# Kernel optimization log

Hardware: AMD Instinct MI355X
Metric: run time of the kernel (lower is better)

Reference implementation:

```python
import jax, jax.numpy as jnp
import numpy as np

N_NODES = 100000
N_EDGES = 1600000
IN_DIM = 128
HID = 64
HEADS = 1
NEG_SLOPE = 0.2


def setup_inputs() -> dict:
    key = jax.random.key(0)
    ks = jax.random.split(key, 12)
    def xavier(k, shape):
        fan_in, fan_out = shape[-2], shape[-1]
        lim = jnp.sqrt(6.0 / (fan_in + fan_out))
        return jax.random.uniform(k, shape, jnp.float32, -lim, lim)
    x = jax.random.normal(ks[0], (N_NODES, IN_DIM), jnp.float32)
    edge_index = jax.random.randint(ks[1], (2, N_EDGES), 0, N_NODES, jnp.int64)
    # layer 0: in 128 -> heads*hid (64)
    W0 = xavier(ks[2], (IN_DIM, HEADS * HID))
    al0 = xavier(ks[3], (1, HEADS, HID))
    ar0 = xavier(ks[4], (1, HEADS, HID))
    # layer 1: in heads*hid (64) -> 64
    W1 = xavier(ks[5], (HEADS * HID, HEADS * HID))
    al1 = xavier(ks[6], (1, HEADS, HID))
    ar1 = xavier(ks[7], (1, HEADS, HID))
    # post_mp: Linear(64,64) -> Linear(64,64)
    Wp1 = xavier(ks[8], (HEADS * HID, HID))
    bp1 = jnp.zeros((HID,), jnp.float32)
    Wp2 = xavier(ks[9], (HID, HID))
    bp2 = jnp.zeros((HID,), jnp.float32)
    return {"x": x, "edge_index": edge_index, "W0": W0, "al0": al0, "ar0": ar0,
            "W1": W1, "al1": al1, "ar1": ar1, "Wp1": Wp1, "bp1": bp1,
            "Wp2": Wp2, "bp2": bp2}


def gat_layer(x, W, att_l, att_r, src, dst, n_nodes):
    H, C = att_l.shape[1], att_l.shape[2]
    # lin_l == lin_r (shared weight), no bias
    xh = (x @ W).reshape(n_nodes, H, C)            # [N,H,C]
    alpha_l = jnp.sum(xh * att_l, axis=-1)         # [N,H]
    alpha_r = jnp.sum(xh * att_r, axis=-1)         # [N,H]
    # per-edge logit: alpha_i (dst) + alpha_j (src)
    a = alpha_l[src] + alpha_r[dst]                # [E,H]
    a = jnp.where(a >= 0, a, NEG_SLOPE * a)        # leaky_relu
    # segment softmax over incoming edges of each dst node
    amax = jax.ops.segment_max(a, dst, num_segments=n_nodes)
    e = jnp.exp(a - amax[dst])
    denom = jax.ops.segment_sum(e, dst, num_segments=n_nodes)
    alpha = e / (denom[dst] + 1e-16)               # [E,H]
    msg = xh[src] * alpha[:, :, None]              # [E,H,C]
    out = jax.ops.segment_sum(msg, dst, num_segments=n_nodes)  # [N,H,C]
    return out.reshape(n_nodes, H * C)


def reference(x, edge_index, W0, al0, ar0, W1, al1, ar1, Wp1, bp1, Wp2, bp2):
    src, dst = edge_index[0], edge_index[1]
    n = x.shape[0]
    h = gat_layer(x, W0, al0, ar0, src, dst, n)
    h = jax.nn.relu(h)
    h = gat_layer(h, W1, al1, ar1, src, dst, n)
    h = jax.nn.relu(h)
    # post_mp (dropout inactive in eval)
    h = h @ Wp1 + bp1
    h = h @ Wp2 + bp2
    return h  # emb=True -> return embedding
```

## Files before the change

### kernel.cpp

```cpp
#include <hip/hip_runtime.h>
#include <math.h>

#define NEG_SLOPE 0.2f
#define CAP 8192

typedef _Float16 half8 __attribute__((ext_vector_type(8)));
typedef _Float16 half4v __attribute__((ext_vector_type(4)));
typedef float float4v __attribute__((ext_vector_type(4)));

__global__ void init_cursor(int* __restrict__ cursor, int NB) {
    int i = blockIdx.x * blockDim.x + threadIdx.x;
    if (i < NB) cursor[i] = i * CAP;
}

__global__ void prep_wt(const float* __restrict__ W0, const float* __restrict__ W1,
                        const float* __restrict__ Wp1, const float* __restrict__ Wp2,
                        _Float16* __restrict__ W0T, _Float16* __restrict__ W1T,
                        _Float16* __restrict__ Wp1T, _Float16* __restrict__ Wp2T) {
    __shared__ float lds[128 * 64];
    const float* src; _Float16* dstp; int K;
    switch (blockIdx.x) {
        case 0: src = W0;  dstp = W0T;  K = 128; break;
        case 1: src = W1;  dstp = W1T;  K = 64;  break;
        case 2: src = Wp1; dstp = Wp1T; K = 64;  break;
        default: src = Wp2; dstp = Wp2T; K = 64; break;
    }
    const int tid = threadIdx.x;
    for (int i = tid; i < K * 64; i += 256) lds[i] = src[i];
    __syncthreads();
    for (int i = tid; i < K * 64; i += 256) {
        int n = i / K, k = i % K;
        dstp[i] = (_Float16)lds[k * 64 + n];
    }
}


__global__ void bucket_bin(const int* __restrict__ src, const int* __restrict__ dst,
                           int* __restrict__ cursor, unsigned int* __restrict__ packed,
                           int E, int NB) {
    __shared__ int h[512];
    const int tid = threadIdx.x;
    for (int t = tid; t < NB; t += 256) h[t] = 0;
    __syncthreads();
    const int base = blockIdx.x * 4096;
    const int lim = min(base + 4096, E);
    for (int i = base + tid; i < lim; i += 256)
        atomicAdd(&h[dst[i] >> 8], 1);
    __syncthreads();
    for (int t = tid; t < NB; t += 256) {
        int c = h[t];
        h[t] = c ? atomicAdd(&cursor[t], c) : 0;
    }
    __syncthreads();
    for (int i = base + tid; i < lim; i += 256) {
        int d = dst[i];
        int pos = atomicAdd(&h[d >> 8], 1);
        packed[pos] = ((unsigned int)(d & 255) << 24) | (unsigned int)src[i];
    }
}

__global__ void bucket_sort(const unsigned int* __restrict__ packed,
                            const int* __restrict__ cursor,
                            int* __restrict__ csr, int* __restrict__ rbeg,
                            int* __restrict__ rend, int N) {
    __shared__ int hist[256], cur[256];
    __shared__ int wsum[4], woff[4];
    const int tid = threadIdx.x, wid = tid >> 6, lane = tid & 63;
    const int b = blockIdx.x;
    const int beg = b * CAP;
    const int end = cursor[b];
    hist[tid] = 0;
    __syncthreads();
    for (int i = beg + tid; i < end; i += 256)
        atomicAdd(&hist[packed[i] >> 24], 1);
    __syncthreads();
    int v = hist[tid];
    int x = v;
    #pragma unroll
    for (int off = 1; off < 64; off <<= 1) {
        int t = __shfl_up(x, off);
        if (lane >= off) x += t;
    }
    if (lane == 63) wsum[wid] = x;
    __syncthreads();
    if (tid == 0) {
        int acc = 0;
        #pragma unroll
        for (int w = 0; w < 4; ++w) { woff[w] = acc; acc += wsum[w]; }
    }
    __syncthreads();
    int excl = woff[wid] + x - v;
    int node = (b << 8) + tid;
    if (node < N) { rbeg[node] = beg + excl; rend[node] = beg + excl + v; }
    cur[tid] = excl;
    __syncthreads();
    for (int i = beg + tid; i < end; i += 256) {
        unsigned int p = packed[i];
        int pos = atomicAdd(&cur[p >> 24], 1);
        csr[beg + pos] = (int)(p & 0xFFFFFFu);
    }
}

template<int K, bool RELU>
__global__ void gemm_node_mfma(const float* __restrict__ X,
                               const _Float16* __restrict__ WT,
                               const float* __restrict__ alw, const float* __restrict__ arw,
                               _Float16* __restrict__ XH, float* __restrict__ AL,
                               float* __restrict__ AR, int N) {
    const int wid = threadIdx.x >> 6, lane = threadIdx.x & 63;
    const int rowbase = blockIdx.x * 64 + wid * 16;
    const int idx16 = lane & 15;
    const int g = lane >> 4;
    const int mrow = rowbase + idx16;
    const bool mvalid = (mrow < N);

    float4v acc[4];
    #pragma unroll
    for (int n = 0; n < 4; ++n) acc[n] = float4v{0.f, 0.f, 0.f, 0.f};

    #pragma unroll
    for (int ks = 0; ks < K / 32; ++ks) {
        const int k0 = ks * 32 + g * 8;
        half8 a = {};
        if (mvalid) {
            const float* xp = X + (size_t)mrow * K + k0;
            float4v lo = *reinterpret_cast<const float4v*>(xp);
            float4v hi = *reinterpret_cast<const float4v*>(xp + 4);
            #pragma unroll
            for (int i = 0; i < 4; ++i) {
                float l = RELU ? fmaxf(lo[i], 0.f) : lo[i];
                float h = RELU ? fmaxf(hi[i], 0.f) : hi[i];
                a[i] = (_Float16)l;
                a[i + 4] = (_Float16)h;
            }
        }
        #pragma unroll
        for (int n = 0; n < 4; ++n) {
            const half8 b = *reinterpret_cast<const half8*>(WT + (size_t)(n * 16 + idx16) * K + k0);
            acc[n] = __builtin_amdgcn_mfma_f32_16x16x32_f16(a, b, acc[n], 0, 0, 0);
        }
    }

    float alv[4], arv[4];
    #pragma unroll
    for (int n = 0; n < 4; ++n) { alv[n] = alw[n * 16 + idx16]; arv[n] = arw[n * 16 + idx16]; }
    #pragma unroll
    for (int r = 0; r < 4; ++r) {
        const int row = rowbase + g * 4 + r;
        if (row < N) {
            float pl = 0.f, pr = 0.f;
            #pragma unroll
            for (int n = 0; n < 4; ++n) {
                float vv = acc[n][r];
                XH[(size_t)row * 64 + n * 16 + idx16] = (_Float16)vv;
                pl = fmaf(vv, alv[n], pl);
                pr = fmaf(vv, arv[n], pr);
            }
            pl += __shfl_xor(pl, 1); pr += __shfl_xor(pr, 1);
            pl += __shfl_xor(pl, 2); pr += __shfl_xor(pr, 2);
            pl += __shfl_xor(pl, 4); pr += __shfl_xor(pr, 4);
            pl += __shfl_xor(pl, 8); pr += __shfl_xor(pr, 8);
            if (idx16 == 0) { AL[row] = pl; AR[row] = pr; }
        }
    }
}


__device__ __forceinline__ void agg_phase(const int* __restrict__ rbeg,
                                          const int* __restrict__ rend,
                                          const int* __restrict__ csr,
                                          const float* __restrict__ ALp,
                                          const float* __restrict__ ARp,
                                          const _Float16* __restrict__ XHp,
                                          _Float16* ts, int nb, int N) {
    const int tid = threadIdx.x;
    const int l = tid & 15, grp = tid >> 4;
    const int node = nb + grp;
    float4v acc = {0.f, 0.f, 0.f, 0.f};
    float inv = 0.0f;
    if (node < N) {
        const int beg = rbeg[node], end = rend[node];
        const float ar = ARp[node];
        float s = 0.f;
        for (int cbeg = beg; cbeg < end; cbeg += 16) {
            const int e = cbeg + l;
            const bool valid = (e < end);
            const int sidx = valid ? csr[e] : 0;
            float a = ALp[sidx] + ar;
            a = (a >= 0.0f) ? a : NEG_SLOPE * a;
            const float ex = valid ? __expf(a) : 0.0f;
            s += ex;
            #pragma unroll
            for (int j = 0; j < 16; ++j) {
                const float wgt = __shfl(ex, j, 16);
                const int si = __shfl(sidx, j, 16);
                const half4v h = *reinterpret_cast<const half4v*>(XHp + (size_t)si * 64 + l * 4);
                acc[0] = fmaf((float)h[0], wgt, acc[0]);
                acc[1] = fmaf((float)h[1], wgt, acc[1]);
                acc[2] = fmaf((float)h[2], wgt, acc[2]);
                acc[3] = fmaf((float)h[3], wgt, acc[3]);
            }
        }
        s += __shfl_xor(s, 1); s += __shfl_xor(s, 2);
        s += __shfl_xor(s, 4); s += __shfl_xor(s, 8);
        inv = 1.0f / (s + 1e-16f);
    }
    half4v o;
    o[0] = (_Float16)fmaxf(acc[0] * inv, 0.f);
    o[1] = (_Float16)fmaxf(acc[1] * inv, 0.f);
    o[2] = (_Float16)fmaxf(acc[2] * inv, 0.f);
    o[3] = (_Float16)fmaxf(acc[3] * inv, 0.f);
    const int hoff = (grp * 128 + ((l * 8) ^ ((grp & 7) << 4))) >> 1;
    *reinterpret_cast<half4v*>(ts + hoff) = o;
    __syncthreads();
}

__device__ __forceinline__ half8 ts_afrag(const _Float16* ts, int row, int kb) {
    return *reinterpret_cast<const half8*>(ts + ((row * 128 + (kb ^ ((row & 7) << 4))) >> 1));
}

__global__ void agg_gemm_mid(const int* __restrict__ rbeg, const int* __restrict__ rend,
                             const int* __restrict__ csr,
                             const float* __restrict__ AL0, const float* __restrict__ AR0,
                             const _Float16* __restrict__ XH0,
                             const _Float16* __restrict__ W1T,
                             const float* __restrict__ al1w, const float* __restrict__ ar1w,
                             _Float16* __restrict__ XH1, float* __restrict__ AL1,
                             float* __restrict__ AR1, int N) {
    __shared__ _Float16 ts[16 * 64];
    const int nb = blockIdx.x * 16;
    agg_phase(rbeg, rend, csr, AL0, AR0, XH0, ts, nb, N);
    if (threadIdx.x >= 64) return;

    const int lane = threadIdx.x;
    const int idx16 = lane & 15, g = lane >> 4;
    float alv[4], arv[4];
    #pragma unroll
    for (int n = 0; n < 4; ++n) { alv[n] = al1w[n * 16 + idx16]; arv[n] = ar1w[n * 16 + idx16]; }

    float4v acc[4];
    #pragma unroll
    for (int n = 0; n < 4; ++n) acc[n] = float4v{0.f, 0.f, 0.f, 0.f};
    #pragma unroll
    for (int ks = 0; ks < 2; ++ks) {
        const half8 a = ts_afrag(ts, idx16, ks * 64 + g * 16);
        const int k0 = ks * 32 + g * 8;
        #pragma unroll
        for (int n = 0; n < 4; ++n) {
            const half8 b = *reinterpret_cast<const half8*>(W1T + (size_t)(n * 16 + idx16) * 64 + k0);
            acc[n] = __builtin_amdgcn_mfma_f32_16x16x32_f16(a, b, acc[n], 0, 0, 0);
        }
    }
    #pragma unroll
    for (int r = 0; r < 4; ++r) {
        const int row = nb + g * 4 + r;
        if (row < N) {
            float pl = 0.f, pr = 0.f;
            #pragma unroll
            for (int n = 0; n < 4; ++n) {
                float vv = acc[n][r];
                XH1[(size_t)row * 64 + n * 16 + idx16] = (_Float16)vv;
                pl = fmaf(vv, alv[n], pl);
                pr = fmaf(vv, arv[n], pr);
            }
            pl += __shfl_xor(pl, 1); pr += __shfl_xor(pr, 1);
            pl += __shfl_xor(pl, 2); pr += __shfl_xor(pr, 2);
            pl += __shfl_xor(pl, 4); pr += __shfl_xor(pr, 4);
            pl += __shfl_xor(pl, 8); pr += __shfl_xor(pr, 8);
            if (idx16 == 0) { AL1[row] = pl; AR1[row] = pr; }
        }
    }
}

__global__ void agg_post(const int* __restrict__ rbeg, const int* __restrict__ rend,
                         const int* __restrict__ csr,
                         const float* __restrict__ AL1, const float* __restrict__ AR1,
                         const _Float16* __restrict__ XH1,
                         const _Float16* __restrict__ Wp1T, const float* __restrict__ bp1,
                         const _Float16* __restrict__ Wp2T, const float* __restrict__ bp2,
                         float* __restrict__ OUT, int N) {
    __shared__ _Float16 ts[16 * 64];
    __shared__ _Float16 tls[16][72];
    const int nb = blockIdx.x * 16;
    agg_phase(rbeg, rend, csr, AL1, AR1, XH1, ts, nb, N);
    if (threadIdx.x >= 64) return;

    const int lane = threadIdx.x;
    const int idx16 = lane & 15, g = lane >> 4;

    float4v acc1[4];
    #pragma unroll
    for (int n = 0; n < 4; ++n) acc1[n] = float4v{0.f, 0.f, 0.f, 0.f};
    #pragma unroll
    for (int ks = 0; ks < 2; ++ks) {
        const half8 a = ts_afrag(ts, idx16, ks * 64 + g * 16);
        const int k0 = ks * 32 + g * 8;
        #pragma unroll
        for (int n = 0; n < 4; ++n) {
            const half8 b = *reinterpret_cast<const half8*>(Wp1T + (size_t)(n * 16 + idx16) * 64 + k0);
            acc1[n] = __builtin_amdgcn_mfma_f32_16x16x32_f16(a, b, acc1[n], 0, 0, 0);
        }
    }
    #pragma unroll
    for (int r = 0; r < 4; ++r)
        #pragma unroll
        for (int n = 0; n < 4; ++n)
            tls[g * 4 + r][n * 16 + idx16] = (_Float16)(acc1[n][r] + bp1[n * 16 + idx16]);

    float4v acc2[4];
    #pragma unroll
    for (int n = 0; n < 4; ++n) acc2[n] = float4v{0.f, 0.f, 0.f, 0.f};
    #pragma unroll
    for (int ks = 0; ks < 2; ++ks) {
        const int k0 = ks * 32 + g * 8;
        const half8 a = *reinterpret_cast<const half8*>(&tls[idx16][k0]);
        #pragma unroll
        for (int n = 0; n < 4; ++n) {
            const half8 b = *reinterpret_cast<const half8*>(Wp2T + (size_t)(n * 16 + idx16) * 64 + k0);
            acc2[n] = __builtin_amdgcn_mfma_f32_16x16x32_f16(a, b, acc2[n], 0, 0, 0);
        }
    }
    #pragma unroll
    for (int r = 0; r < 4; ++r) {
        const int row = nb + g * 4 + r;
        if (row < N) {
            #pragma unroll
            for (int n = 0; n < 4; ++n)
                OUT[(size_t)row * 64 + n * 16 + idx16] = acc2[n][r] + bp2[n * 16 + idx16];
        }
    }
}

extern "C" void kernel_launch(void* const* d_in, const int* in_sizes, int n_in,
                              void* d_out, int out_size, void* d_ws, size_t ws_size,
                              hipStream_t stream) {
    const float* x   = (const float*)d_in[0];
    const int*   ei  = (const int*)d_in[1];
    const float* W0  = (const float*)d_in[2];
    const float* al0 = (const float*)d_in[3];
    const float* ar0 = (const float*)d_in[4];
    const float* W1  = (const float*)d_in[5];
    const float* al1 = (const float*)d_in[6];
    const float* ar1 = (const float*)d_in[7];
    const float* Wp1 = (const float*)d_in[8];
    const float* bp1 = (const float*)d_in[9];
    const float* Wp2 = (const float*)d_in[10];
    const float* bp2 = (const float*)d_in[11];
    float* out = (float*)d_out;

    const int N = in_sizes[0] / 128;
    const int E = in_sizes[1] / 2;
    const int* src = ei;
    const int* dst = ei + E;
    const int NB = (N + 255) >> 8;

    char* w = (char*)d_ws;
    _Float16* XH0  = (_Float16*)w;     w += sizeof(_Float16) * (size_t)N * 64;
    _Float16* XH1  = (_Float16*)w;     w += sizeof(_Float16) * (size_t)N * 64;
    float*  AL0    = (float*)w;        w += sizeof(float) * N;
    float*  AR0    = (float*)w;        w += sizeof(float) * N;
    float*  AL1    = (float*)w;        w += sizeof(float) * N;
    float*  AR1    = (float*)w;        w += sizeof(float) * N;
    int*    rbeg   = (int*)w;          w += sizeof(int) * N;
    int*    rend   = (int*)w;          w += sizeof(int) * N;
    int*    csr    = (int*)w;          w += sizeof(int) * (size_t)NB * CAP;
    unsigned int* packed = (unsigned int*)w; w += sizeof(unsigned int) * (size_t)NB * CAP;
    int*    cursor = (int*)w;          w += sizeof(int) * 512;
    _Float16* W0T  = (_Float16*)w;     w += sizeof(_Float16) * 128 * 64;
    _Float16* W1T  = (_Float16*)w;     w += sizeof(_Float16) * 64 * 64;
    _Float16* Wp1T = (_Float16*)w;     w += sizeof(_Float16) * 64 * 64;
    _Float16* Wp2T = (_Float16*)w;

    dim3 blk(256);
    const int gn64 = (N + 63) / 64;
    const int gn16 = (N + 15) / 16;
    const int geb  = (E + 4095) / 4096;

    prep_wt<<<4, blk, 0, stream>>>(W0, W1, Wp1, Wp2, W0T, W1T, Wp1T, Wp2T);
    init_cursor<<<2, blk, 0, stream>>>(cursor, NB);
    bucket_bin<<<geb, blk, 0, stream>>>(src, dst, cursor, packed, E, NB);
    bucket_sort<<<NB, blk, 0, stream>>>(packed, cursor, csr, rbeg, rend, N);

    gemm_node_mfma<128, false><<<gn64, blk, 0, stream>>>(x, W0T, al0, ar0, XH0, AL0, AR0, N);

    agg_gemm_mid<<<gn16, blk, 0, stream>>>(rbeg, rend, csr, AL0, AR0, XH0,
                                           W1T, al1, ar1, XH1, AL1, AR1, N);

    agg_post<<<gn16, blk, 0, stream>>>(rbeg, rend, csr, AL1, AR1, XH1,
                                       Wp1T, bp1, Wp2T, bp2, out, N);
}
```

Measured before the change: 162.9 us.

## Fuse setup kernels and co-schedule edge binning with layer-0 GEMM

Merges cursor init into the weight-transpose kernel. The edge bucket-binning pass and the layer-0 node GEMM now share a single launch, split by block index, so the two independent phases run concurrently and the launch count drops. Binning caches dst indices in registers rather than reading them twice. Row begin/end offsets are packed into one int2 array so each node needs one load. The risk is added register pressure from the dreg array and uneven block mixing within the fused launch.

```diff
diff --git a/kernel.cpp b/kernel.cpp
--- a/kernel.cpp
+++ b/kernel.cpp
@@ -8,15 +8,16 @@
 typedef _Float16 half4v __attribute__((ext_vector_type(4)));
 typedef float float4v __attribute__((ext_vector_type(4)));
 
-__global__ void init_cursor(int* __restrict__ cursor, int NB) {
-    int i = blockIdx.x * blockDim.x + threadIdx.x;
-    if (i < NB) cursor[i] = i * CAP;
-}
-
-__global__ void prep_wt(const float* __restrict__ W0, const float* __restrict__ W1,
-                        const float* __restrict__ Wp1, const float* __restrict__ Wp2,
-                        _Float16* __restrict__ W0T, _Float16* __restrict__ W1T,
-                        _Float16* __restrict__ Wp1T, _Float16* __restrict__ Wp2T) {
+__global__ void setup_misc(const float* __restrict__ W0, const float* __restrict__ W1,
+                           const float* __restrict__ Wp1, const float* __restrict__ Wp2,
+                           _Float16* __restrict__ W0T, _Float16* __restrict__ W1T,
+                           _Float16* __restrict__ Wp1T, _Float16* __restrict__ Wp2T,
+                           int* __restrict__ cursor, int NB) {
+    const int tid = threadIdx.x;
+    if (blockIdx.x == 4) {
+        for (int t = tid; t < NB; t += 256) cursor[t] = t * CAP;
+        return;
+    }
     __shared__ float lds[128 * 64];
     const float* src; _Float16* dstp; int K;
     switch (blockIdx.x) {
@@ -25,7 +26,6 @@
         case 2: src = Wp1; dstp = Wp1T; K = 64;  break;
         default: src = Wp2; dstp = Wp2T; K = 64; break;
     }
-    const int tid = threadIdx.x;
     for (int i = tid; i < K * 64; i += 256) lds[i] = src[i];
     __syncthreads();
     for (int i = tid; i < K * 64; i += 256) {
@@ -34,81 +34,45 @@
     }
 }
 
-
-__global__ void bucket_bin(const int* __restrict__ src, const int* __restrict__ dst,
-                           int* __restrict__ cursor, unsigned int* __restrict__ packed,
-                           int E, int NB) {
+__device__ __forceinline__ void bin_body(const int* __restrict__ src,
+                                         const int* __restrict__ dst,
+                                         int* __restrict__ cursor,
+                                         unsigned int* __restrict__ packed,
+                                         int E, int NB, int bid) {
     __shared__ int h[512];
     const int tid = threadIdx.x;
     for (int t = tid; t < NB; t += 256) h[t] = 0;
     __syncthreads();
-    const int base = blockIdx.x * 4096;
+    const int base = bid * 4096;
     const int lim = min(base + 4096, E);
-    for (int i = base + tid; i < lim; i += 256)
-        atomicAdd(&h[dst[i] >> 8], 1);
+    int dreg[16];
+    int cnt = 0;
+    for (int i = base + tid; i < lim; i += 256) dreg[cnt++] = dst[i];
+    for (int k = 0; k < cnt; ++k) atomicAdd(&h[dreg[k] >> 8], 1);
     __syncthreads();
     for (int t = tid; t < NB; t += 256) {
         int c = h[t];
         h[t] = c ? atomicAdd(&cursor[t], c) : 0;
     }
     __syncthreads();
+    cnt = 0;
     for (int i = base + tid; i < lim; i += 256) {
-        int d = dst[i];
+        int d = dreg[cnt++];
+        int s = src[i];
         int pos = atomicAdd(&h[d >> 8], 1);
-        packed[pos] = ((unsigned int)(d & 255) << 24) | (unsigned int)src[i];
-    }
-}
-
-__global__ void bucket_sort(const unsigned int* __restrict__ packed,
-                            const int* __restrict__ cursor,
-                            int* __restrict__ csr, int* __restrict__ rbeg,
-                            int* __restrict__ rend, int N) {
-    __shared__ int hist[256], cur[256];
-    __shared__ int wsum[4], woff[4];
-    const int tid = threadIdx.x, wid = tid >> 6, lane = tid & 63;
-    const int b = blockIdx.x;
-    const int beg = b * CAP;
-    const int end = cursor[b];
-    hist[tid] = 0;
-    __syncthreads();
-    for (int i = beg + tid; i < end; i += 256)
-        atomicAdd(&hist[packed[i] >> 24], 1);
-    __syncthreads();
-    int v = hist[tid];
-    int x = v;
-    #pragma unroll
-    for (int off = 1; off < 64; off <<= 1) {
-        int t = __shfl_up(x, off);
-        if (lane >= off) x += t;
-    }
-    if (lane == 63) wsum[wid] = x;
-    __syncthreads();
-    if (tid == 0) {
-        int acc = 0;
-        #pragma unroll
-        for (int w = 0; w < 4; ++w) { woff[w] = acc; acc += wsum[w]; }
-    }
-    __syncthreads();
-    int excl = woff[wid] + x - v;
-    int node = (b << 8) + tid;
-    if (node < N) { rbeg[node] = beg + excl; rend[node] = beg + excl + v; }
-    cur[tid] = excl;
-    __syncthreads();
-    for (int i = beg + tid; i < end; i += 256) {
-        unsigned int p = packed[i];
-        int pos = atomicAdd(&cur[p >> 24], 1);
-        csr[beg + pos] = (int)(p & 0xFFFFFFu);
-    }
-}
-
-template<int K, bool RELU>
-__global__ void gemm_node_mfma(const float* __restrict__ X,
-                               const _Float16* __restrict__ WT,
-                               const float* __restrict__ alw, const float* __restrict__ arw,
-                               _Float16* __restrict__ XH, float* __restrict__ AL,
-                               float* __restrict__ AR, int N) {
+        packed[pos] = ((unsigned int)(d & 255) << 24) | (unsigned int)s;
+    }
+}
+
+__device__ __forceinline__ void gemm0_body(const float* __restrict__ X,
+                                           const _Float16* __restrict__ WT,
+                                           const float* __restrict__ alw,
+                                           const float* __restrict__ arw,
+                                           _Float16* __restrict__ XH,
+                                           float* __restrict__ AL, float* __restrict__ AR,
+                                           int N, int bid) {
     const int wid = threadIdx.x >> 6, lane = threadIdx.x & 63;
-    const int rowbase = blockIdx.x * 64 + wid * 16;
+    const int rowbase = bid * 64 + wid * 16;
     const int idx16 = lane & 15;
     const int g = lane >> 4;
     const int mrow = rowbase + idx16;
@@ -119,24 +83,22 @@
     for (int n = 0; n < 4; ++n) acc[n] = float4v{0.f, 0.f, 0.f, 0.f};
 
     #pragma unroll
-    for (int ks = 0; ks < K / 32; ++ks) {
+    for (int ks = 0; ks < 4; ++ks) {
         const int k0 = ks * 32 + g * 8;
         half8 a = {};
         if (mvalid) {
-            const float* xp = X + (size_t)mrow * K + k0;
+            const float* xp = X + (size_t)mrow * 128 + k0;
             float4v lo = *reinterpret_cast<const float4v*>(xp);
             float4v hi = *reinterpret_cast<const float4v*>(xp + 4);
             #pragma unroll
             for (int i = 0; i < 4; ++i) {
-                float l = RELU ? fmaxf(lo[i], 0.f) : lo[i];
-                float h = RELU ? fmaxf(hi[i], 0.f) : hi[i];
-                a[i] = (_Float16)l;
-                a[i + 4] = (_Float16)h;
+                a[i] = (_Float16)lo[i];
+                a[i + 4] = (_Float16)hi[i];
             }
         }
         #pragma unroll
         for (int n = 0; n < 4; ++n) {
-            const half8 b = *reinterpret_cast<const half8*>(WT + (size_t)(n * 16 + idx16) * K + k0);
+            const half8 b = *reinterpret_cast<const half8*>(WT + (size_t)(n * 16 + idx16) * 128 + k0);
             acc[n] = __builtin_amdgcn_mfma_f32_16x16x32_f16(a, b, acc[n], 0, 0, 0);
         }
     }
@@ -165,9 +127,63 @@
     }
 }
 
-
-__device__ __forceinline__ void agg_phase(const int* __restrict__ rbeg,
-                                          const int* __restrict__ rend,
+__global__ void gemm0_and_bin(const float* __restrict__ X,
+                              const _Float16* __restrict__ W0T,
+                              const float* __restrict__ alw, const float* __restrict__ arw,
+                              _Float16* __restrict__ XH0, float* __restrict__ AL0,
+                              float* __restrict__ AR0,
+                              const int* __restrict__ src, const int* __restrict__ dst,
+                              int* __restrict__ cursor, unsigned int* __restrict__ packed,
+                              int N, int E, int NB, int geb) {
+    if ((int)blockIdx.x < geb)
+        bin_body(src, dst, cursor, packed, E, NB, blockIdx.x);
+    else
+        gemm0_body(X, W0T, alw, arw, XH0, AL0, AR0, N, blockIdx.x - geb);
+}
+
+__global__ void bucket_sort(const unsigned int* __restrict__ packed,
+                            const int* __restrict__ cursor,
+                            int* __restrict__ csr, int2* __restrict__ rr, int N) {
+    __shared__ int hist[256], cur[256];
+    __shared__ int wsum[4], woff[4];
+    const int tid = threadIdx.x, wid = tid >> 6, lane = tid & 63;
+    const int b = blockIdx.x;
+    const int beg = b * CAP;
+    const int end = cursor[b];
+    hist[tid] = 0;
+    __syncthreads();
+    for (int i = beg + tid; i < end; i += 256)
+        atomicAdd(&hist[packed[i] >> 24], 1);
+    __syncthreads();
+    int v = hist[tid];
+    int x = v;
+    #pragma unroll
+    for (int off = 1; off < 64; off <<= 1) {
+        int t = __shfl_up(x, off);
+        if (lane >= off) x += t;
+    }
+    if (lane == 63) wsum[wid] = x;
+    __syncthreads();
+    if (tid == 0) {
+        int acc = 0;
+        #pragma unroll
+        for (int w = 0; w < 4; ++w) { woff[w] = acc; acc += wsum[w]; }
+    }
+    __syncthreads();
+    int excl = woff[wid] + x - v;
+    int node = (b << 8) + tid;
+    if (node < N) rr[node] = make_int2(beg + excl, v);
+    cur[tid] = excl;
+    __syncthreads();
+    for (int i = beg + tid; i < end; i += 256) {
+        unsigned int p = packed[i];
+        int pos = atomicAdd(&cur[p >> 24], 1);
+        csr[beg + pos] = (int)(p & 0xFFFFFFu);
+    }
+}
+
+
+__device__ __forceinline__ void agg_phase(const int2* __restrict__ rr,
                                           const int* __restrict__ csr,
                                           const float* __restrict__ ALp,
                                           const float* __restrict__ ARp,
@@ -179,7 +195,8 @@
     float4v acc = {0.f, 0.f, 0.f, 0.f};
     float inv = 0.0f;
     if (node < N) {
-        const int beg = rbeg[node], end = rend[node];
+        const int2 r = rr[node];
+        const int beg = r.x, end = r.x + r.y;
         const float ar = ARp[node];
         float s = 0.f;
         for (int cbeg = beg; cbeg < end; cbeg += 16) {
@@ -219,8 +236,7 @@
     return *reinterpret_cast<const half8*>(ts + ((row * 128 + (kb ^ ((row & 7) << 4))) >> 1));
 }
 
-__global__ void agg_gemm_mid(const int* __restrict__ rbeg, const int* __restrict__ rend,
-                             const int* __restrict__ csr,
+__global__ void agg_gemm_mid(const int2* __restrict__ rr, const int* __restrict__ csr,
                              const float* __restrict__ AL0, const float* __restrict__ AR0,
                              const _Float16* __restrict__ XH0,
                              const _Float16* __restrict__ W1T,
@@ -229,7 +245,7 @@
                              float* __restrict__ AR1, int N) {
     __shared__ _Float16 ts[16 * 64];
     const int nb = blockIdx.x * 16;
-    agg_phase(rbeg, rend, csr, AL0, AR0, XH0, ts, nb, N);
+    agg_phase(rr, csr, AL0, AR0, XH0, ts, nb, N);
     if (threadIdx.x >= 64) return;
 
     const int lane = threadIdx.x;
@@ -272,8 +288,7 @@
     }
 }
 
-__global__ void agg_post(const int* __restrict__ rbeg, const int* __restrict__ rend,
-                         const int* __restrict__ csr,
+__global__ void agg_post(const int2* __restrict__ rr, const int* __restrict__ csr,
                          const float* __restrict__ AL1, const float* __restrict__ AR1,
                          const _Float16* __restrict__ XH1,
                          const _Float16* __restrict__ Wp1T, const float* __restrict__ bp1,
@@ -282,7 +297,7 @@
     __shared__ _Float16 ts[16 * 64];
     __shared__ _Float16 tls[16][72];
     const int nb = blockIdx.x * 16;
-    agg_phase(rbeg, rend, csr, AL1, AR1, XH1, ts, nb, N);
+    agg_phase(rr, csr, AL1, AR1, XH1, ts, nb, N);
     if (threadIdx.x >= 64) return;
 
     const int lane = threadIdx.x;
@@ -361,8 +376,7 @@
     float*  AR0    = (float*)w;        w += sizeof(float) * N;
     float*  AL1    = (float*)w;        w += sizeof(float) * N;
     float*  AR1    = (float*)w;        w += sizeof(float) * N;
-    int*    rbeg   = (int*)w;          w += sizeof(int) * N;
-    int*    rend   = (int*)w;          w += sizeof(int) * N;
+    int2*   rr     = (int2*)w;         w += sizeof(int2) * N;
     int*    csr    = (int*)w;          w += sizeof(int) * (size_t)NB * CAP;
     unsigned int* packed = (unsigned int*)w; w += sizeof(unsigned int) * (size_t)NB * CAP;
     int*    cursor = (int*)w;          w += sizeof(int) * 512;
@@ -376,16 +390,18 @@
     const int gn16 = (N + 15) / 16;
     const int geb  = (E + 4095) / 4096;
 
-    prep_wt<<<4, blk, 0, stream>>>(W0, W1, Wp1, Wp2, W0T, W1T, Wp1T, Wp2T);
-    init_cursor<<<2, blk, 0, stream>>>(cursor, NB);
-    bucket_bin<<<geb, blk, 0, stream>>>(src, dst, cursor, packed, E, NB);
-    bucket_sort<<<NB, blk, 0, stream>>>(packed, cursor, csr, rbeg, rend, N);
-
-    gemm_node_mfma<128, false><<<gn64, blk, 0, stream>>>(x, W0T, al0, ar0, XH0, AL0, AR0, N);
-
-    agg_gemm_mid<<<gn16, blk, 0, stream>>>(rbeg, rend, csr, AL0, AR0, XH0,
+    setup_misc<<<5, blk, 0, stream>>>(W0, W1, Wp1, Wp2, W0T, W1T, Wp1T, Wp2T,
+                                      cursor, NB);
+
+    gemm0_and_bin<<<geb + gn64, blk, 0, stream>>>(x, W0T, al0, ar0, XH0, AL0, AR0,
+                                                  src, dst, cursor, packed,
+                                                  N, E, NB, geb);
+
+    bucket_sort<<<NB, blk, 0, stream>>>(packed, cursor, csr, rr, N);
+
+    agg_gemm_mid<<<gn16, blk, 0, stream>>>(rr, csr, AL0, AR0, XH0,
                                            W1T, al1, ar1, XH1, AL1, AR1, N);
 
-    agg_post<<<gn16, blk, 0, stream>>>(rbeg, rend, csr, AL1, AR1, XH1,
+    agg_post<<<gn16, blk, 0, stream>>>(rr, csr, AL1, AR1, XH1,
                                        Wp1T, bp1, Wp2T, bp2, out, N);
 }
```

Result: faster. 150.5 us (-7.6%).
